# Kernel tuning notes

Hardware: AMD Instinct MI355X
Metric: run time of the kernel (lower is better)

Reference implementation:

```python
import jax, jax.numpy as jnp
import numpy as np

N = 100000


def gcn_conv(x, W, b, src, dst, deg_inv_sqrt, n):
    # PyG GCNConv: h = D^{-1/2} (A + I) D^{-1/2} (x W) + b
    h = x @ W  # [N, out]
    norm = deg_inv_sqrt[src] * deg_inv_sqrt[dst]  # [E+N]
    msgs = h[src] * norm[:, None]  # gathered + scaled messages
    out = jax.ops.segment_sum(msgs, dst, num_segments=n)
    return out + b


def _self_loops_and_norm(edge_index, n):
    src, dst = edge_index[0], edge_index[1]
    loop = jnp.arange(n, dtype=edge_index.dtype)
    src = jnp.concatenate([src, loop])
    dst = jnp.concatenate([dst, loop])
    deg = jax.ops.segment_sum(jnp.ones_like(dst, dtype=jnp.float32), dst, num_segments=n)
    deg_inv_sqrt = jnp.where(deg > 0, jax.lax.rsqrt(jnp.maximum(deg, 1.0)), 0.0)
    return src, dst, deg_inv_sqrt


def setup_inputs() -> dict:
    key = jax.random.key(0)
    k1, k2, k3, k4 = jax.random.split(key, 4)
    nfeat, nhid, nclass = 512, 256, 40
    E = 3200000
    x = jax.random.normal(k1, (N, nfeat), dtype=jnp.float32)
    edge_index = jax.random.randint(k2, (2, E), 0, N, dtype=jnp.int64)
    # Glorot-style init for GCNConv weights, zero bias (PyG default)
    W1 = jax.random.normal(k3, (nfeat, nhid), dtype=jnp.float32) / np.sqrt(nfeat)
    b1 = jnp.zeros((nhid,), dtype=jnp.float32)
    W2 = jax.random.normal(k4, (nhid, nclass), dtype=jnp.float32) / np.sqrt(nhid)
    b2 = jnp.zeros((nclass,), dtype=jnp.float32)
    return {"x": x, "W1": W1, "b1": b1, "W2": W2, "b2": b2, "edge_index": edge_index}


def reference(x, W1, b1, W2, b2, edge_index):
    src, dst, dis = _self_loops_and_norm(edge_index, N)
    h = gcn_conv(x, W1, b1, src, dst, dis, N)
    h = jax.nn.relu(h)
    # dropout(p=0.5) is identity in eval mode
    h = gcn_conv(h, W2, b2, src, dst, dis, N)
    return jax.nn.log_softmax(h, axis=1)
```

## Files before the change

kernel.cpp:

```cpp
#include <hip/hip_runtime.h>
#include <math.h>

#define NFEAT 512
#define NHID  256
#define NCLASS 40
#define NBUCK 782
#define BCAP  5120
#define PCHUNK 8192

typedef __attribute__((ext_vector_type(8))) short short8;
typedef __attribute__((ext_vector_type(4))) float f32x4;


__device__ __forceinline__ float bflo(unsigned u) {
    union { unsigned i; float f; } x; x.i = u << 16; return x.f;
}
__device__ __forceinline__ float bfhi(unsigned u) {
    union { unsigned i; float f; } x; x.i = u & 0xffff0000u; return x.f;
}
__device__ __forceinline__ unsigned short f2bf(float f) {
    union { float f; unsigned i; } x; x.f = f;
    unsigned r = x.i + 0x7fffu + ((x.i >> 16) & 1u);
    return (unsigned short)(r >> 16);
}
__device__ __forceinline__ unsigned pack2(float a, float b) {
    return (unsigned)f2bf(a) | ((unsigned)f2bf(b) << 16);
}


__global__ __launch_bounds__(256) void partcast_k(const float* __restrict__ W1,
                                                  unsigned short* __restrict__ WT,
                                                  const int* __restrict__ ei,
                                                  int* bucketCnt,
                                                  unsigned* __restrict__ binned, int E) {
    __shared__ unsigned staged[PCHUNK];
    __shared__ int hist[NBUCK];
    __shared__ int lofs[NBUCK];
    __shared__ int sbase[NBUCK];
    __shared__ int lcur[NBUCK];
    __shared__ int wsum[256];
    int bid = blockIdx.x;
    int t = threadIdx.x;
    if (bid < (NFEAT * NHID) / 256) {
        int idx = bid * 256 + t;
        int k = idx >> 8;
        int nn = idx & 255;
        WT[(size_t)nn * NFEAT + k] = f2bf(W1[idx]);
        return;
    }
    int pb = bid - (NFEAT * NHID) / 256;
    int beg = pb * PCHUNK;
    int end = beg + PCHUNK; if (end > E) end = E;

    for (int b = t; b < NBUCK; b += 256) hist[b] = 0;
    __syncthreads();
    for (int e = beg + t; e < end; e += 256) {
        int d = ei[(size_t)E + e];
        atomicAdd(&hist[d >> 7], 1);
    }
    __syncthreads();
    int v[4];
    int s0 = 0;
#pragma unroll
    for (int r = 0; r < 4; ++r) {
        int idx = t * 4 + r;
        v[r] = (idx < NBUCK) ? hist[idx] : 0;
        s0 += v[r];
    }
    wsum[t] = s0;
    __syncthreads();
    for (int off = 1; off < 256; off <<= 1) {
        int add = (t >= off) ? wsum[t - off] : 0;
        __syncthreads();
        wsum[t] += add;
        __syncthreads();
    }
    int excl = wsum[t] - s0;
#pragma unroll
    for (int r = 0; r < 4; ++r) {
        int idx = t * 4 + r;
        if (idx < NBUCK) { lofs[idx] = excl; lcur[idx] = excl; }
        excl += v[r];
    }
    __syncthreads();
    for (int b = t; b < NBUCK; b += 256) {
        int h = hist[b];
        if (h) sbase[b] = atomicAdd(&bucketCnt[b], h);
    }
    for (int e = beg + t; e < end; e += 256) {
        int s = ei[e];
        int d = ei[(size_t)E + e];
        int b = d >> 7;
        int p = atomicAdd(&lcur[b], 1);
        staged[p] = ((unsigned)s << 7) | (unsigned)(d & 127);
    }
    __syncthreads();
    int w = t >> 6, lane = t & 63;
    for (int b = w; b < NBUCK; b += 4) {
        int h = hist[b];
        if (!h) continue;
        int lo = lofs[b];
        size_t gb = (size_t)b * BCAP + sbase[b];
        for (int l = lane; l < h; l += 64)
            binned[gb + l] = staged[lo + l];
    }
}


__global__ __launch_bounds__(1024) void bscan_k(const int* __restrict__ bucketCnt,
                                                int* __restrict__ bbase,
                                                int* __restrict__ offs, int n, int E) {
    __shared__ int sd[1024];
    int t = threadIdx.x;
    int v = (t < NBUCK) ? bucketCnt[t] : 0;
    sd[t] = v;
    __syncthreads();
    for (int off = 1; off < 1024; off <<= 1) {
        int add = (t >= off) ? sd[t - off] : 0;
        __syncthreads();
        sd[t] += add;
        __syncthreads();
    }
    if (t < NBUCK) bbase[t] = sd[t] - v;
    if (t == 0) offs[n] = E;
}


__global__ __launch_bounds__(512) void fill2_k(const unsigned* __restrict__ binned,
                                               const int* __restrict__ bucketCnt,
                                               const int* __restrict__ bbase,
                                               int* __restrict__ offs,
                                               float* __restrict__ dis,
                                               int* __restrict__ csrs, int n) {
    __shared__ int h128[128];
    __shared__ int sd[128];
    __shared__ int lcur[128];
    int b = blockIdx.x;
    int t = threadIdx.x;
    int node0 = b << 7;
    int cbt = bucketCnt[b];
    size_t base_in = (size_t)b * BCAP;
    int gbase = bbase[b];
    if (t < 128) h128[t] = 0;
    __syncthreads();
    for (int e = t; e < cbt; e += 512) {
        unsigned u = binned[base_in + e];
        atomicAdd(&h128[u & 127], 1);
    }
    __syncthreads();
    int v = (t < 128) ? h128[t] : 0;
    if (t < 128) sd[t] = v;
    __syncthreads();
    for (int off = 1; off < 128; off <<= 1) {
        int add = (t < 128 && t >= off) ? sd[t - off] : 0;
        __syncthreads();
        if (t < 128) sd[t] += add;
        __syncthreads();
    }
    if (t < 128) {
        int excl = sd[t] - v;
        int nd = node0 + t;
        if (nd < n) {
            offs[nd] = gbase + excl;
            dis[nd] = rsqrtf((float)v + 1.0f);
        }
        lcur[t] = gbase + excl;
    }
    __syncthreads();
    for (int e = t; e < cbt; e += 512) {
        unsigned u = binned[base_in + e];
        int pos = atomicAdd(&lcur[u & 127], 1);
        csrs[pos] = (int)(u >> 7);
    }
}


__global__ __launch_bounds__(512) void gemm1_k(const float* __restrict__ X,
                                               const unsigned short* __restrict__ WT,
                                               const float* __restrict__ dis,
                                               unsigned short* __restrict__ H, int M) {
    __shared__ unsigned short as[128][72];
    __shared__ unsigned short bs[256][72];
    int t = threadIdx.x;
    int lane = t & 63;
    int w = t >> 6;
    int wm = w >> 2;
    int wn = w & 3;
    int m0 = blockIdx.x * 128;
    int quad = lane >> 4;
    int r16 = lane & 15;

    f32x4 acc[4][4];
#pragma unroll
    for (int a = 0; a < 4; ++a)
#pragma unroll
        for (int b = 0; b < 4; ++b) acc[a][b] = (f32x4){0.f, 0.f, 0.f, 0.f};

    for (int k0 = 0; k0 < NFEAT; k0 += 64) {
        {
            int m = t >> 2;
            int c = (t & 3) * 16;
            int gi = m0 + m;
            float4 v0, v1, v2, v3;
            if (gi < M) {
                const float4* p = (const float4*)(X + (size_t)gi * NFEAT + k0 + c);
                v0 = p[0]; v1 = p[1]; v2 = p[2]; v3 = p[3];
            } else {
                v0 = v1 = v2 = v3 = make_float4(0.f, 0.f, 0.f, 0.f);
            }
            uint4 p0, p1;
            p0.x = pack2(v0.x, v0.y); p0.y = pack2(v0.z, v0.w);
            p0.z = pack2(v1.x, v1.y); p0.w = pack2(v1.z, v1.w);
            p1.x = pack2(v2.x, v2.y); p1.y = pack2(v2.z, v2.w);
            p1.z = pack2(v3.x, v3.y); p1.w = pack2(v3.z, v3.w);
            *(uint4*)&as[m][c] = p0;
            *(uint4*)&as[m][c + 8] = p1;
        }
        {
            int row = t >> 1;
            int ch = (t & 1) * 32;
            const uint4* p = (const uint4*)(WT + (size_t)row * NFEAT + k0 + ch);
#pragma unroll
            for (int c = 0; c < 4; ++c) {
                uint4 q = p[c];
                *(uint4*)&bs[row][ch + c * 8] = q;
            }
        }
        __syncthreads();
#pragma unroll
        for (int ks = 0; ks < 64; ks += 32) {
            short8 af[4], bfr[4];
#pragma unroll
            for (int sm = 0; sm < 4; ++sm)
                af[sm] = *(const short8*)&as[wm * 64 + sm * 16 + r16][ks + quad * 8];
#pragma unroll
            for (int sn = 0; sn < 4; ++sn)
                bfr[sn] = *(const short8*)&bs[wn * 64 + sn * 16 + r16][ks + quad * 8];
#pragma unroll
            for (int sm = 0; sm < 4; ++sm)
#pragma unroll
                for (int sn = 0; sn < 4; ++sn)
                    acc[sm][sn] = __builtin_amdgcn_mfma_f32_16x16x32_bf16(
                        af[sm], bfr[sn], acc[sm][sn], 0, 0, 0);
        }
        __syncthreads();
    }
#pragma unroll
    for (int sm = 0; sm < 4; ++sm) {
#pragma unroll
        for (int rr = 0; rr < 4; ++rr) {
            int row = m0 + wm * 64 + sm * 16 + quad * 4 + rr;
            if (row < M) {
                float dsc = dis[row];
#pragma unroll
                for (int sn = 0; sn < 4; ++sn) {
                    int col = wn * 64 + sn * 16 + r16;
                    H[(size_t)row * NHID + col] = f2bf(acc[sm][sn][rr] * dsc);
                }
            }
        }
    }
}


__global__ __launch_bounds__(256) void agg1h_k(const unsigned short* __restrict__ Hb,
                                               const int* __restrict__ offs,
                                               const int* __restrict__ csrs,
                                               const float* __restrict__ dis,
                                               const float* __restrict__ b1,
                                               unsigned short* __restrict__ outb,
                                               int n, int f0u) {
    int lane = threadIdx.x & 63;
    int i = blockIdx.x * 4 + (threadIdx.x >> 6);
    if (i >= n) return;
    const unsigned* Hv = (const unsigned*)Hb;
    int col = f0u + lane;
    float a0 = 0.f, a1 = 0.f;
    int beg = offs[i], end = offs[i + 1];
    int e = beg;
    {
        int c[16]; unsigned g[16];
        for (; e + 16 <= end; e += 16) {
#pragma unroll
            for (int u = 0; u < 16; ++u) c[u] = csrs[e + u];
#pragma unroll
            for (int u = 0; u < 16; ++u) g[u] = Hv[(size_t)c[u] * 128 + col];
#pragma unroll
            for (int u = 0; u < 16; ++u) {
                a0 += bflo(g[u]); a1 += bfhi(g[u]);
            }
        }
        if (e < end) {
#pragma unroll
            for (int u = 0; u < 16; ++u)
                c[u] = (e + u < end) ? csrs[e + u] : i;
#pragma unroll
            for (int u = 0; u < 16; ++u) g[u] = Hv[(size_t)c[u] * 128 + col];
#pragma unroll
            for (int u = 0; u < 16; ++u) {
                float sel = (e + u < end) ? 1.f : 0.f;
                a0 = fmaf(sel, bflo(g[u]), a0); a1 = fmaf(sel, bfhi(g[u]), a1);
            }
        }
    }
    unsigned v = Hv[(size_t)i * 128 + col];
    a0 += bflo(v); a1 += bfhi(v);
    float di = dis[i];
    float2 bb = ((const float2*)b1)[col];
    a0 = fmaxf(fmaf(a0, di, bb.x), 0.f);
    a1 = fmaxf(fmaf(a1, di, bb.y), 0.f);
    ((unsigned*)outb)[(size_t)i * 128 + col] = pack2(a0, a1);
}


__global__ __launch_bounds__(256) void gemm2_k(const unsigned short* __restrict__ Ab,
                                               const float* __restrict__ W2,
                                               const float* __restrict__ dis,
                                               unsigned short* __restrict__ H2b, int M) {
    __shared__ float w2t[NCLASS][260];
    int t = threadIdx.x;
    for (int idx = t; idx < NHID * NCLASS; idx += 256) {
        int k = idx / NCLASS;
        int j = idx - k * NCLASS;
        w2t[j][k] = W2[idx];
    }
    __syncthreads();
    int i = blockIdx.x * 32 + (t >> 3);
    if (i >= M) return;
    int j0 = (t & 7) * 5;
    const uint2* arow = (const uint2*)(Ab + (size_t)i * NHID);
    float acc[5] = {0.f, 0.f, 0.f, 0.f, 0.f};
#pragma unroll 4
    for (int c = 0; c < 64; ++c) {
        uint2 v = arow[c];
        float a0 = bflo(v.x), a1 = bfhi(v.x), a2 = bflo(v.y), a3 = bfhi(v.y);
        int k = c * 4;
#pragma unroll
        for (int jj = 0; jj < 5; ++jj) {
            float4 q = *(const float4*)&w2t[j0 + jj][k];
            acc[jj] += a0 * q.x + a1 * q.y + a2 * q.z + a3 * q.w;
        }
    }
    float di = dis[i];
#pragma unroll
    for (int jj = 0; jj < 5; ++jj)
        H2b[(size_t)i * 64 + j0 + jj] = f2bf(acc[jj] * di);
    if ((t & 7) < 3)
        ((uint4*)(H2b + (size_t)i * 64 + 40))[t & 7] = make_uint4(0u, 0u, 0u, 0u);
}


__global__ __launch_bounds__(256) void agg2_k(const unsigned short* __restrict__ H2b,
                                              const int* __restrict__ offs,
                                              const int* __restrict__ csrs,
                                              const float* __restrict__ dis,
                                              const float* __restrict__ b2,
                                              float* __restrict__ out, int n) {
    int lane = threadIdx.x & 63;
    int i = blockIdx.x * 4 + (threadIdx.x >> 6);
    if (i >= n) return;
    const uint2* Hv = (const uint2*)H2b;
    int slot = lane >> 4;
    int r16 = lane & 15;
    float a0 = 0.f, a1 = 0.f, a2 = 0.f, a3 = 0.f;
    int beg = offs[i], end = offs[i + 1];
    int e = beg;
    {
        int c[8]; uint2 g[8];
        for (; e + 32 <= end; e += 32) {
#pragma unroll
            for (int u = 0; u < 8; ++u) c[u] = csrs[e + u * 4 + slot];
#pragma unroll
            for (int u = 0; u < 8; ++u) g[u] = Hv[(size_t)c[u] * 16 + r16];
#pragma unroll
            for (int u = 0; u < 8; ++u) {
                a0 += bflo(g[u].x); a1 += bfhi(g[u].x);
                a2 += bflo(g[u].y); a3 += bfhi(g[u].y);
            }
        }
        if (e < end) {
#pragma unroll
            for (int u = 0; u < 8; ++u) {
                int idx = e + u * 4 + slot;
                c[u] = (idx < end) ? csrs[idx] : i;
            }
#pragma unroll
            for (int u = 0; u < 8; ++u) g[u] = Hv[(size_t)c[u] * 16 + r16];
#pragma unroll
            for (int u = 0; u < 8; ++u) {
                float sel = (e + u * 4 + slot < end) ? 1.f : 0.f;
                a0 = fmaf(sel, bflo(g[u].x), a0); a1 = fmaf(sel, bfhi(g[u].x), a1);
                a2 = fmaf(sel, bflo(g[u].y), a2); a3 = fmaf(sel, bfhi(g[u].y), a3);
            }
        }
    }
    if (slot == 0) {
        uint2 v = Hv[(size_t)i * 16 + r16];
        a0 += bflo(v.x); a1 += bfhi(v.x);
        a2 += bflo(v.y); a3 += bfhi(v.y);
    }
    a0 += __shfl_xor(a0, 16, 64); a0 += __shfl_xor(a0, 32, 64);
    a1 += __shfl_xor(a1, 16, 64); a1 += __shfl_xor(a1, 32, 64);
    a2 += __shfl_xor(a2, 16, 64); a2 += __shfl_xor(a2, 32, 64);
    a3 += __shfl_xor(a3, 16, 64); a3 += __shfl_xor(a3, 32, 64);
    float di = dis[i];
    bool act = (r16 < 10);
    float4 bb = act ? ((const float4*)b2)[r16] : make_float4(0.f, 0.f, 0.f, 0.f);
    a0 = fmaf(a0, di, bb.x); a1 = fmaf(a1, di, bb.y);
    a2 = fmaf(a2, di, bb.z); a3 = fmaf(a3, di, bb.w);
    float m = act ? fmaxf(fmaxf(a0, a1), fmaxf(a2, a3)) : -INFINITY;
#pragma unroll
    for (int off = 8; off > 0; off >>= 1) m = fmaxf(m, __shfl_xor(m, off, 16));
    float s = act ? (expf(a0 - m) + expf(a1 - m) + expf(a2 - m) + expf(a3 - m)) : 0.f;
#pragma unroll
    for (int off = 8; off > 0; off >>= 1) s += __shfl_xor(s, off, 16);
    float ls = m + logf(s);
    if (lane < 10) {
        float4 o = make_float4(a0 - ls, a1 - ls, a2 - ls, a3 - ls);
        ((float4*)(out + (size_t)i * NCLASS))[lane] = o;
    }
}


extern "C" void kernel_launch(void* const* d_in, const int* in_sizes, int n_in,
                              void* d_out, int out_size, void* d_ws, size_t ws_size,
                              hipStream_t stream) {
    const float* x  = (const float*)d_in[0];
    const float* W1 = (const float*)d_in[1];
    const float* b1 = (const float*)d_in[2];
    const float* W2 = (const float*)d_in[3];
    const float* b2 = (const float*)d_in[4];
    const int*   ei = (const int*)d_in[5];

    const int N = in_sizes[0] / NFEAT;
    const int E = in_sizes[5] / 2;

    size_t off = 0;
    auto alloc = [&](size_t bytes) { size_t o = off; off += (bytes + 255) & ~(size_t)255; return o; };
    char* ws = (char*)d_ws;
    int*            offs    = (int*)           (ws + alloc((size_t)(N + 1) * 4));
    float*          dis     = (float*)         (ws + alloc((size_t)N * 4));
    int*            bcnt    = (int*)           (ws + alloc((size_t)NBUCK * 4));
    int*            bbase   = (int*)           (ws + alloc((size_t)NBUCK * 4));
    unsigned*       binned  = (unsigned*)      (ws + alloc((size_t)NBUCK * BCAP * 4));
    int*            csrs    = (int*)           (ws + alloc((size_t)E * 4));
    unsigned short* wT      = (unsigned short*)(ws + alloc((size_t)NFEAT * NHID * 2));
    unsigned short* h1b     = (unsigned short*)(ws + alloc((size_t)N * NHID * 2));
    unsigned short* a1b     = (unsigned short*)(ws + alloc((size_t)N * NHID * 2));
    unsigned short* h2b     = (unsigned short*)(ws + alloc((size_t)N * 64 * 2));
    float*          out     = (float*)d_out;

    int npart = (E + PCHUNK - 1) / PCHUNK;

    hipMemsetAsync(bcnt, 0, (size_t)NBUCK * 4, stream);
    partcast_k<<<(NFEAT * NHID) / 256 + npart, 256, 0, stream>>>(W1, wT, ei, bcnt, binned, E);
    bscan_k<<<1, 1024, 0, stream>>>(bcnt, bbase, offs, N, E);
    fill2_k<<<NBUCK, 512, 0, stream>>>(binned, bcnt, bbase, offs, dis, csrs, N);
    gemm1_k<<<(N + 127) / 128, 512, 0, stream>>>(x, wT, dis, h1b, N);
    agg1h_k<<<(N + 3) / 4, 256, 0, stream>>>(h1b, offs, csrs, dis, b1, a1b, N, 0);
    agg1h_k<<<(N + 3) / 4, 256, 0, stream>>>(h1b, offs, csrs, dis, b1, a1b, N, 64);
    gemm2_k<<<(N + 31) / 32, 256, 0, stream>>>(a1b, W2, dis, h2b, N);
    agg2_k<<<(N + 3) / 4, 256, 0, stream>>>(h2b, offs, csrs, dis, b2, out, N);
}
```

Baseline: 755.3 us.

## Use bf16 MFMA with hi/lo split weights for second-layer GEMM

The second GEMM (N×256 by 256×40) now runs on MFMA bf16 16x16x32 instructions instead of scalar FP32 FMAs over an LDS-transposed W2. W2 is pre-transposed and split into bf16 high and low parts inside the partition/cast kernel, so accuracy stays near FP32 at the cost of two MFMAs per tile. Each block handles 64 rows, and the padded columns 40-47 are computed as zeros. This removes the per-block W2 transpose and the scalar inner loop, but adds one extra block to the setup kernel.

```diff
diff --git a/kernel.cpp b/kernel.cpp
--- a/kernel.cpp
+++ b/kernel.cpp
@@ -23,6 +23,9 @@
     unsigned r = x.i + 0x7fffu + ((x.i >> 16) & 1u);
     return (unsigned short)(r >> 16);
 }
+__device__ __forceinline__ float bf2f(unsigned short h) {
+    union { unsigned i; float f; } x; x.i = (unsigned)h << 16; return x.f;
+}
 __device__ __forceinline__ unsigned pack2(float a, float b) {
     return (unsigned)f2bf(a) | ((unsigned)f2bf(b) << 16);
 }
@@ -30,6 +33,8 @@
 
 __global__ __launch_bounds__(256) void partcast_k(const float* __restrict__ W1,
                                                   unsigned short* __restrict__ WT,
+                                                  const float* __restrict__ W2,
+                                                  unsigned short* __restrict__ WT2,
                                                   const int* __restrict__ ei,
                                                   int* bucketCnt,
                                                   unsigned* __restrict__ binned, int E) {
@@ -48,7 +53,18 @@
         WT[(size_t)nn * NFEAT + k] = f2bf(W1[idx]);
         return;
     }
-    int pb = bid - (NFEAT * NHID) / 256;
+    if (bid == (NFEAT * NHID) / 256) {
+        for (int idx = t; idx < 96 * 256; idx += 256) {
+            int j2 = idx >> 8;
+            int k = idx & 255;
+            int j = (j2 < 48) ? j2 : j2 - 48;
+            float v = (j < NCLASS) ? W2[k * NCLASS + j] : 0.f;
+            unsigned short hi = f2bf(v);
+            WT2[idx] = (j2 < 48) ? hi : f2bf(v - bf2f(hi));
+        }
+        return;
+    }
+    int pb = bid - (NFEAT * NHID) / 256 - 1;
     int beg = pb * PCHUNK;
     int end = beg + PCHUNK; if (end > E) end = E;
 
@@ -314,39 +330,57 @@
 
 
 __global__ __launch_bounds__(256) void gemm2_k(const unsigned short* __restrict__ Ab,
-                                               const float* __restrict__ W2,
+                                               const unsigned short* __restrict__ WT2,
                                                const float* __restrict__ dis,
                                                unsigned short* __restrict__ H2b, int M) {
-    __shared__ float w2t[NCLASS][260];
+    __shared__ unsigned short wt2s[96][264];
     int t = threadIdx.x;
-    for (int idx = t; idx < NHID * NCLASS; idx += 256) {
-        int k = idx / NCLASS;
-        int j = idx - k * NCLASS;
-        w2t[j][k] = W2[idx];
-    }
-    __syncthreads();
-    int i = blockIdx.x * 32 + (t >> 3);
-    if (i >= M) return;
-    int j0 = (t & 7) * 5;
-    const uint2* arow = (const uint2*)(Ab + (size_t)i * NHID);
-    float acc[5] = {0.f, 0.f, 0.f, 0.f, 0.f};
-#pragma unroll 4
-    for (int c = 0; c < 64; ++c) {
-        uint2 v = arow[c];
-        float a0 = bflo(v.x), a1 = bfhi(v.x), a2 = bflo(v.y), a3 = bfhi(v.y);
-        int k = c * 4;
-#pragma unroll
-        for (int jj = 0; jj < 5; ++jj) {
-            float4 q = *(const float4*)&w2t[j0 + jj][k];
-            acc[jj] += a0 * q.x + a1 * q.y + a2 * q.z + a3 * q.w;
-        }
-    }
-    float di = dis[i];
-#pragma unroll
-    for (int jj = 0; jj < 5; ++jj)
-        H2b[(size_t)i * 64 + j0 + jj] = f2bf(acc[jj] * di);
-    if ((t & 7) < 3)
-        ((uint4*)(H2b + (size_t)i * 64 + 40))[t & 7] = make_uint4(0u, 0u, 0u, 0u);
+    int lane = t & 63;
+    int w = t >> 6;
+    int quad = lane >> 4;
+    int r16 = lane & 15;
+    for (int idx = t; idx < 96 * 32; idx += 256) {
+        int r = idx >> 5;
+        int c = idx & 31;
+        *(uint4*)&wt2s[r][c * 8] = ((const uint4*)(WT2 + (size_t)r * 256))[c];
+    }
+    __syncthreads();
+    int row0 = blockIdx.x * 64 + w * 16;
+    int gr = row0 + r16;
+    f32x4 acc[3];
+#pragma unroll
+    for (int sn = 0; sn < 3; ++sn) acc[sn] = (f32x4){0.f, 0.f, 0.f, 0.f};
+#pragma unroll
+    for (int ks = 0; ks < 8; ++ks) {
+        short8 af;
+        if (gr < M)
+            af = *(const short8*)(Ab + (size_t)gr * NHID + ks * 32 + quad * 8);
+        else
+            af = (short8){0, 0, 0, 0, 0, 0, 0, 0};
+#pragma unroll
+        for (int sn = 0; sn < 3; ++sn) {
+            short8 bhi = *(const short8*)&wt2s[sn * 16 + r16][ks * 32 + quad * 8];
+            short8 blo = *(const short8*)&wt2s[48 + sn * 16 + r16][ks * 32 + quad * 8];
+            acc[sn] = __builtin_amdgcn_mfma_f32_16x16x32_bf16(af, bhi, acc[sn], 0, 0, 0);
+            acc[sn] = __builtin_amdgcn_mfma_f32_16x16x32_bf16(af, blo, acc[sn], 0, 0, 0);
+        }
+    }
+#pragma unroll
+    for (int rr = 0; rr < 4; ++rr) {
+        int row = row0 + quad * 4 + rr;
+        if (row < M) {
+            float dsc = dis[row];
+#pragma unroll
+            for (int sn = 0; sn < 3; ++sn)
+                H2b[(size_t)row * 64 + sn * 16 + r16] = f2bf(acc[sn][rr] * dsc);
+        }
+    }
+    if (lane < 32) {
+        int row = row0 + r16;
+        if (row < M)
+            *(uint4*)&H2b[(size_t)row * 64 + 48 + (lane >> 4) * 8] =
+                make_uint4(0u, 0u, 0u, 0u);
+    }
 }
 
 
@@ -445,6 +479,7 @@
     unsigned*       binned  = (unsigned*)      (ws + alloc((size_t)NBUCK * BCAP * 4));
     int*            csrs    = (int*)           (ws + alloc((size_t)E * 4));
     unsigned short* wT      = (unsigned short*)(ws + alloc((size_t)NFEAT * NHID * 2));
+    unsigned short* wT2     = (unsigned short*)(ws + alloc((size_t)96 * 256 * 2));
     unsigned short* h1b     = (unsigned short*)(ws + alloc((size_t)N * NHID * 2));
     unsigned short* a1b     = (unsigned short*)(ws + alloc((size_t)N * NHID * 2));
     unsigned short* h2b     = (unsigned short*)(ws + alloc((size_t)N * 64 * 2));
@@ -453,12 +488,13 @@
     int npart = (E + PCHUNK - 1) / PCHUNK;
 
     hipMemsetAsync(bcnt, 0, (size_t)NBUCK * 4, stream);
-    partcast_k<<<(NFEAT * NHID) / 256 + npart, 256, 0, stream>>>(W1, wT, ei, bcnt, binned, E);
+    partcast_k<<<(NFEAT * NHID) / 256 + 1 + npart, 256, 0, stream>>>(W1, wT, W2, wT2, ei,
+                                                                     bcnt, binned, E);
     bscan_k<<<1, 1024, 0, stream>>>(bcnt, bbase, offs, N, E);
     fill2_k<<<NBUCK, 512, 0, stream>>>(binned, bcnt, bbase, offs, dis, csrs, N);
     gemm1_k<<<(N + 127) / 128, 512, 0, stream>>>(x, wT, dis, h1b, N);
     agg1h_k<<<(N + 3) / 4, 256, 0, stream>>>(h1b, offs, csrs, dis, b1, a1b, N, 0);
     agg1h_k<<<(N + 3) / 4, 256, 0, stream>>>(h1b, offs, csrs, dis, b1, a1b, N, 64);
-    gemm2_k<<<(N + 31) / 32, 256, 0, stream>>>(a1b, W2, dis, h2b, N);
+    gemm2_k<<<(N + 63) / 64, 256, 0, stream>>>(a1b, wT2, dis, h2b, N);
     agg2_k<<<(N + 3) / 4, 256, 0, stream>>>(h2b, offs, csrs, dis, b2, out, N);
 }
```

New measurement: 715.8 us. 5.2% less time.
